# Kernel optimization log

Hardware: AMD Instinct MI355X
Metric: run time of the kernel (lower is better)

The kernel has to match this reference:

```python
import jax, jax.numpy as jnp
import numpy as np
import math

NUM_REG_TOKENS = 0  # encoder.num_register_tokens
EPS = 1e-12         # matches torch F.normalize eps


def _l2norm(x):
    # F.normalize(x, dim=-1): x / max(||x||, eps)
    n = jnp.sqrt(jnp.sum(x * x, axis=-1, keepdims=True))
    return x / jnp.maximum(n, EPS)


def setup_inputs() -> dict:
    key = jax.random.key(0)
    k1, k2 = jax.random.split(key)
    L, N, S, T, D = 3, 8, 4, 1370, 768  # 3 interested layers, T = 1 + 37^2 patches
    q_feats = jax.random.normal(k1, (L, N, T, D), dtype=jnp.float32)
    s_feats = jax.random.normal(k2, (L, N * S, T, D), dtype=jnp.float32)
    return {"q_feats": q_feats, "s_feats": s_feats}


def reference(q_feats, s_feats):
    # fuse_feature: mean over stacked interested layers
    xq = jnp.mean(q_feats, axis=0)   # [N, T, D]
    xs = jnp.mean(s_feats, axis=0)   # [N*S, T, D]
    N = xq.shape[0]
    Q = xq.shape[1] - 1 - NUM_REG_TOKENS
    side = int(math.isqrt(Q))
    # drop class (+register) tokens
    xq = xq[:, 1 + NUM_REG_TOKENS:, :]                 # [N, Q, D]
    xs = xs[:, 1 + NUM_REG_TOKENS:, :]                 # [N*S, Q, D]
    xs = xs.reshape(N, -1, xs.shape[-1])               # [N, S*Q, D]
    xq = _l2norm(xq)
    xs = _l2norm(xs)
    # cosine distance + 1-NN min over support tokens
    sim = jnp.einsum('nqd,nsd->nqs', xq, xs)           # [N, Q, S*Q]
    dist = jnp.min(1.0 - sim, axis=-1)                 # [N, Q]
    return dist.reshape(N, 1, side, side)
```

## Files before the change

kernel.cpp:

```cpp
#include <hip/hip_runtime.h>
#include <hip/hip_bf16.h>

typedef __attribute__((ext_vector_type(4))) float f32x4;
typedef __attribute__((ext_vector_type(8))) int i32x8;

#define T_TOK 1370
#define DDIM  768
#define SCV   1369
#define SCP   1408
#define MQP   1536
#define NB    8
#define NSLAB 32
#define NST   22
#define NMT   6

#define MEMFENCE asm volatile("" ::: "memory")
#define BARRIER  do { __builtin_amdgcn_s_barrier(); MEMFENCE; } while (0)
#define LGKM0    asm volatile("s_waitcnt lgkmcnt(0)" ::: "memory")

#define GLOAD_LDS16(g, l)                                                     \
  __builtin_amdgcn_global_load_lds(                                           \
      (const __attribute__((address_space(1))) unsigned int*)(g),             \
      (__attribute__((address_space(3))) unsigned int*)(l), 16, 0, 0)

extern "C" __global__ __launch_bounds__(192) void prep_kernel(
    const float* __restrict__ src, unsigned char* __restrict__ dst,
    size_t lstride)
{
  const int row  = blockIdx.x;
  const int slab = blockIdx.y;
  const int t    = threadIdx.x;
  unsigned char* drow = dst + ((size_t)slab * gridDim.x + row) * DDIM;
  if (row >= SCV) {
    reinterpret_cast<unsigned int*>(drow)[t] = 0u;
    return;
  }
  const float* base = src + ((size_t)slab * T_TOK + row + 1) * DDIM;
  float4 a = reinterpret_cast<const float4*>(base)[t];
  float4 b = reinterpret_cast<const float4*>(base + lstride)[t];
  float4 c = reinterpret_cast<const float4*>(base + 2 * lstride)[t];
  const float k3 = 1.0f / 3.0f;
  float4 m;
  m.x = (a.x + b.x + c.x) * k3;
  m.y = (a.y + b.y + c.y) * k3;
  m.z = (a.z + b.z + c.z) * k3;
  m.w = (a.w + b.w + c.w) * k3;
  float ss = m.x * m.x + m.y * m.y + m.z * m.z + m.w * m.w;
  #pragma unroll
  for (int d = 1; d < 64; d <<= 1) ss += __shfl_xor(ss, d);
  __shared__ float wsum[3];
  if ((t & 63) == 0) wsum[t >> 6] = ss;
  __syncthreads();
  float tot = wsum[0] + wsum[1] + wsum[2];
  float rn = 1.0f / fmaxf(sqrtf(tot), 1e-12f);
  int pk = __builtin_amdgcn_cvt_pk_fp8_f32(m.x * rn, m.y * rn, 0, false);
  pk = __builtin_amdgcn_cvt_pk_fp8_f32(m.z * rn, m.w * rn, pk, true);
  reinterpret_cast<unsigned int*>(drow)[t] = (unsigned int)pk;
}

extern "C" __global__ __launch_bounds__(512, 2) void simmax_kernel(
    const unsigned char* __restrict__ xq,
    const unsigned char* __restrict__ xs,
    float* __restrict__ part)
{
  const int flat = blockIdx.x;
  const int swz  = (flat & 7) * (NMT * NST) + (flat >> 3);
  const int n    = swz / (NMT * NST);
  const int idx  = swz - n * (NMT * NST);
  const int mt   = idx % NMT;
  const int st   = idx / NMT;

  const int tid  = threadIdx.x;
  const int lane = tid & 63;
  const int w    = tid >> 6;
  const int wr   = w >> 2;
  const int wcn  = w & 3;
  const int l15  = lane & 15, l4 = lane >> 4;

  __shared__ unsigned char Abuf[2][32768];
  __shared__ unsigned char Bbuf[3][32768];

  const unsigned char* gA = xq + ((size_t)n * MQP + (size_t)mt * 256) * DDIM;
  const unsigned char* gB = xs + ((size_t)n * 4 * SCP + (size_t)st * 256) * DDIM;

  int goff[4], ldso[4];
  #pragma unroll
  for (int i = 0; i < 4; ++i) {
    int c = w * 4 + i;
    int r = c * 8 + (lane >> 3);
    goff[i] = r * DDIM + (((lane & 7) ^ (r & 7)) << 4);
    ldso[i] = c * 1024;
  }

  int aoff[8], boff[4];
  #pragma unroll
  for (int mf = 0; mf < 8; ++mf) {
    int row = wr * 128 + mf * 16 + l15;
    aoff[mf] = row * 128 + ((((l4 << 1) ^ (row & 7))) << 4);
  }
  #pragma unroll
  for (int nf = 0; nf < 4; ++nf) {
    int row = wcn * 64 + nf * 16 + l15;
    boff[nf] = row * 128 + ((((l4 << 1) ^ (row & 7))) << 4);
  }

  f32x4 acc[8][4];
  {
    f32x4 zz = {0.f, 0.f, 0.f, 0.f};
    #pragma unroll
    for (int a = 0; a < 8; ++a)
      #pragma unroll
      for (int b = 0; b < 4; ++b) acc[a][b] = zz;
  }

  #define ISSUE_A(KT)                                                        \
    do {                                                                     \
      const unsigned char* ga_ = gA + (KT) * 128;                            \
      unsigned char* la_ = Abuf[(KT) & 1];                                   \
      _Pragma("unroll") for (int i = 0; i < 4; ++i)                          \
        GLOAD_LDS16(ga_ + goff[i], la_ + ldso[i]);                           \
    } while (0)
  #define ISSUE_B(KT)                                                        \
    do {                                                                     \
      const unsigned char* gb_ = gB + (KT) * 128;                            \
      unsigned char* lb_ = Bbuf[(KT) % 3];                                   \
      _Pragma("unroll") for (int i = 0; i < 4; ++i)                          \
        GLOAD_LDS16(gb_ + goff[i], lb_ + ldso[i]);                           \
    } while (0)

  #define READ_FRAG(PTR, OFF, DST)                                           \
    do {                                                                     \
      int4 lo_ = *reinterpret_cast<const int4*>((PTR) + (OFF));              \
      int4 hi_ = *reinterpret_cast<const int4*>((PTR) + ((OFF) ^ 16));       \
      DST = i32x8{lo_.x, lo_.y, lo_.z, lo_.w, hi_.x, hi_.y, hi_.z, hi_.w};   \
    } while (0)

  ISSUE_A(0);
  ISSUE_B(0);
  ISSUE_B(1);
  asm volatile("s_waitcnt vmcnt(4)" ::: "memory");
  BARRIER;

  for (int kt = 0; kt < 6; ++kt) {
    if (kt < 5) ISSUE_A(kt + 1);
    if (kt < 4) ISSUE_B(kt + 2);

    const char* Ab = reinterpret_cast<const char*>(Abuf[kt & 1]);
    const char* Bb = reinterpret_cast<const char*>(Bbuf[kt % 3]);

    i32x8 bfr[4], af0, af1;
    #pragma unroll
    for (int nf = 0; nf < 4; ++nf) READ_FRAG(Bb, boff[nf], bfr[nf]);
    READ_FRAG(Ab, aoff[0], af0);
    READ_FRAG(Ab, aoff[1], af1);
    BARRIER; LGKM0;
    __builtin_amdgcn_s_setprio(1);
    #pragma unroll
    for (int nf = 0; nf < 4; ++nf) {
      acc[0][nf] = __builtin_amdgcn_mfma_scale_f32_16x16x128_f8f6f4(
          af0, bfr[nf], acc[0][nf], 0, 0, 0, 127, 0, 127);
      acc[1][nf] = __builtin_amdgcn_mfma_scale_f32_16x16x128_f8f6f4(
          af1, bfr[nf], acc[1][nf], 0, 0, 0, 127, 0, 127);
    }
    __builtin_amdgcn_s_setprio(0);
    BARRIER;

    #pragma unroll
    for (int p = 1; p < 4; ++p) {
      i32x8 afa, afb;
      READ_FRAG(Ab, aoff[2 * p], afa);
      READ_FRAG(Ab, aoff[2 * p + 1], afb);
      if (p == 3) {
        if (kt < 4)       asm volatile("s_waitcnt vmcnt(4)" ::: "memory");
        else if (kt == 4) asm volatile("s_waitcnt vmcnt(0)" ::: "memory");
      }
      BARRIER; LGKM0;
      __builtin_amdgcn_s_setprio(1);
      #pragma unroll
      for (int nf = 0; nf < 4; ++nf) {
        acc[2 * p][nf] = __builtin_amdgcn_mfma_scale_f32_16x16x128_f8f6f4(
            afa, bfr[nf], acc[2 * p][nf], 0, 0, 0, 127, 0, 127);
        acc[2 * p + 1][nf] = __builtin_amdgcn_mfma_scale_f32_16x16x128_f8f6f4(
            afb, bfr[nf], acc[2 * p + 1][nf], 0, 0, 0, 127, 0, 127);
      }
      __builtin_amdgcn_s_setprio(0);
      BARRIER;
    }
  }

  bool colv[4];
  #pragma unroll
  for (int nf = 0; nf < 4; ++nf) {
    int col = st * 256 + wcn * 64 + nf * 16 + l15;
    int within = col - (col / SCP) * SCP;
    colv[nf] = within < SCV;
  }

  float rm[8][4];
  #pragma unroll
  for (int mf = 0; mf < 8; ++mf)
    #pragma unroll
    for (int j = 0; j < 4; ++j) {
      float v = -1e30f;
      #pragma unroll
      for (int nf = 0; nf < 4; ++nf)
        if (colv[nf]) v = fmaxf(v, acc[mf][nf][j]);
      rm[mf][j] = v;
    }

  #pragma unroll
  for (int msk = 1; msk < 16; msk <<= 1)
    #pragma unroll
    for (int mf = 0; mf < 8; ++mf)
      #pragma unroll
      for (int j = 0; j < 4; ++j)
        rm[mf][j] = fmaxf(rm[mf][j], __shfl_xor(rm[mf][j], msk));

  __syncthreads();
  float* sfold = reinterpret_cast<float*>(&Abuf[0][0]);
  if (l15 == 0) {
    #pragma unroll
    for (int mf = 0; mf < 8; ++mf)
      #pragma unroll
      for (int j = 0; j < 4; ++j) {
        int r = wr * 128 + mf * 16 + l4 * 4 + j;
        sfold[wcn * 256 + r] = rm[mf][j];
      }
  }
  __syncthreads();
  if (tid < 256) {
    float v = fmaxf(fmaxf(sfold[tid], sfold[256 + tid]),
                    fmaxf(sfold[512 + tid], sfold[768 + tid]));
    part[((size_t)n * NST + st) * MQP + (size_t)mt * 256 + tid] = v;
  }
}

extern "C" __global__ void finalize_kernel(const float* __restrict__ part,
                                           float* __restrict__ out) {
  int i = blockIdx.x * 256 + threadIdx.x;
  if (i >= NB * SCV) return;
  int n = i / SCV, q = i - n * SCV;
  const float* p = part + (size_t)n * NST * MQP + q;
  float m = p[0];
  #pragma unroll 4
  for (int g = 1; g < NST; ++g) m = fmaxf(m, p[(size_t)g * MQP]);
  out[i] = 1.0f - m;
}

extern "C" void kernel_launch(void* const* d_in, const int* in_sizes, int n_in,
                              void* d_out, int out_size, void* d_ws, size_t ws_size,
                              hipStream_t stream) {
  const float* q_feats = (const float*)d_in[0];
  const float* s_feats = (const float*)d_in[1];
  float* out = (float*)d_out;

  char* ws = (char*)d_ws;
  const size_t xq_bytes = (size_t)NB * MQP * DDIM;
  const size_t xs_bytes = (size_t)NSLAB * SCP * DDIM;
  unsigned char* xq = (unsigned char*)ws;
  unsigned char* xs = (unsigned char*)(ws + xq_bytes);
  float* part       = (float*)(ws + xq_bytes + xs_bytes);

  prep_kernel<<<dim3(MQP, NB), 192, 0, stream>>>(
      q_feats, xq, (size_t)NB * T_TOK * DDIM);
  prep_kernel<<<dim3(SCP, NSLAB), 192, 0, stream>>>(
      s_feats, xs, (size_t)NSLAB * T_TOK * DDIM);
  simmax_kernel<<<dim3(NB * NMT * NST), 512, 0, stream>>>(xq, xs, part);
  finalize_kernel<<<dim3((NB * SCV + 255) / 256), 256, 0, stream>>>(part, out);
}
```

Baseline: 193.0 us.

## Shrink query tile to 192 rows and use one barrier per k-step

The query (A) tile per block shrinks from 256 to 192 rows, so there are 8 M-tiles instead of 6. Each wave now holds 6x4 accumulators instead of 8x4, and the A LDS buffers get smaller. The k-loop is also restructured: all six A fragments are read up front and the 24 MFMAs run back-to-back, with a single vmcnt wait and barrier at the end of each k-step instead of four barrier-separated sub-phases. This aims to cut synchronization stalls and register pressure, possibly raising occupancy, at the cost of less B reuse per block, more blocks and more B reloads from memory.

```diff
diff --git a/kernel.cpp b/kernel.cpp
--- a/kernel.cpp
+++ b/kernel.cpp
@@ -12,11 +12,10 @@
 #define NB    8
 #define NSLAB 32
 #define NST   22
-#define NMT   6
+#define NMT   8
 
 #define MEMFENCE asm volatile("" ::: "memory")
 #define BARRIER  do { __builtin_amdgcn_s_barrier(); MEMFENCE; } while (0)
-#define LGKM0    asm volatile("s_waitcnt lgkmcnt(0)" ::: "memory")
 
 #define GLOAD_LDS16(g, l)                                                     \
   __builtin_amdgcn_global_load_lds(                                           \
@@ -77,25 +76,32 @@
   const int wcn  = w & 3;
   const int l15  = lane & 15, l4 = lane >> 4;
 
-  __shared__ unsigned char Abuf[2][32768];
+  __shared__ unsigned char Abuf[2][24576];
   __shared__ unsigned char Bbuf[3][32768];
 
-  const unsigned char* gA = xq + ((size_t)n * MQP + (size_t)mt * 256) * DDIM;
+  const unsigned char* gA = xq + ((size_t)n * MQP + (size_t)mt * 192) * DDIM;
   const unsigned char* gB = xs + ((size_t)n * 4 * SCP + (size_t)st * 256) * DDIM;
 
-  int goff[4], ldso[4];
+  int agoff[3], aldso[3], bgoff[4], bldso[4];
+  #pragma unroll
+  for (int i = 0; i < 3; ++i) {
+    int c = w * 3 + i;
+    int r = c * 8 + (lane >> 3);
+    agoff[i] = r * DDIM + (((lane & 7) ^ (r & 7)) << 4);
+    aldso[i] = c * 1024;
+  }
   #pragma unroll
   for (int i = 0; i < 4; ++i) {
     int c = w * 4 + i;
     int r = c * 8 + (lane >> 3);
-    goff[i] = r * DDIM + (((lane & 7) ^ (r & 7)) << 4);
-    ldso[i] = c * 1024;
-  }
-
-  int aoff[8], boff[4];
-  #pragma unroll
-  for (int mf = 0; mf < 8; ++mf) {
-    int row = wr * 128 + mf * 16 + l15;
+    bgoff[i] = r * DDIM + (((lane & 7) ^ (r & 7)) << 4);
+    bldso[i] = c * 1024;
+  }
+
+  int aoff[6], boff[4];
+  #pragma unroll
+  for (int mf = 0; mf < 6; ++mf) {
+    int row = wr * 96 + mf * 16 + l15;
     aoff[mf] = row * 128 + ((((l4 << 1) ^ (row & 7))) << 4);
   }
   #pragma unroll
@@ -104,11 +110,11 @@
     boff[nf] = row * 128 + ((((l4 << 1) ^ (row & 7))) << 4);
   }
 
-  f32x4 acc[8][4];
+  f32x4 acc[6][4];
   {
     f32x4 zz = {0.f, 0.f, 0.f, 0.f};
     #pragma unroll
-    for (int a = 0; a < 8; ++a)
+    for (int a = 0; a < 6; ++a)
       #pragma unroll
       for (int b = 0; b < 4; ++b) acc[a][b] = zz;
   }
@@ -117,15 +123,15 @@
     do {                                                                     \
       const unsigned char* ga_ = gA + (KT) * 128;                            \
       unsigned char* la_ = Abuf[(KT) & 1];                                   \
-      _Pragma("unroll") for (int i = 0; i < 4; ++i)                          \
-        GLOAD_LDS16(ga_ + goff[i], la_ + ldso[i]);                           \
+      _Pragma("unroll") for (int i = 0; i < 3; ++i)                          \
+        GLOAD_LDS16(ga_ + agoff[i], la_ + aldso[i]);                         \
     } while (0)
   #define ISSUE_B(KT)                                                        \
     do {                                                                     \
       const unsigned char* gb_ = gB + (KT) * 128;                            \
       unsigned char* lb_ = Bbuf[(KT) % 3];                                   \
       _Pragma("unroll") for (int i = 0; i < 4; ++i)                          \
-        GLOAD_LDS16(gb_ + goff[i], lb_ + ldso[i]);                           \
+        GLOAD_LDS16(gb_ + bgoff[i], lb_ + bldso[i]);                         \
     } while (0)
 
   #define READ_FRAG(PTR, OFF, DST)                                           \
@@ -137,55 +143,36 @@
 
   ISSUE_A(0);
   ISSUE_B(0);
+  MEMFENCE;
   ISSUE_B(1);
   asm volatile("s_waitcnt vmcnt(4)" ::: "memory");
   BARRIER;
 
   for (int kt = 0; kt < 6; ++kt) {
-    if (kt < 5) ISSUE_A(kt + 1);
-    if (kt < 4) ISSUE_B(kt + 2);
+    if (kt + 1 < 6) ISSUE_A(kt + 1);
+    MEMFENCE;
+    if (kt + 2 < 6) ISSUE_B(kt + 2);
 
     const char* Ab = reinterpret_cast<const char*>(Abuf[kt & 1]);
     const char* Bb = reinterpret_cast<const char*>(Bbuf[kt % 3]);
-
-    i32x8 bfr[4], af0, af1;
+    i32x8 bfr[4], af[6];
     #pragma unroll
     for (int nf = 0; nf < 4; ++nf) READ_FRAG(Bb, boff[nf], bfr[nf]);
-    READ_FRAG(Ab, aoff[0], af0);
-    READ_FRAG(Ab, aoff[1], af1);
-    BARRIER; LGKM0;
+    #pragma unroll
+    for (int mf = 0; mf < 6; ++mf) READ_FRAG(Ab, aoff[mf], af[mf]);
+
     __builtin_amdgcn_s_setprio(1);
     #pragma unroll
-    for (int nf = 0; nf < 4; ++nf) {
-      acc[0][nf] = __builtin_amdgcn_mfma_scale_f32_16x16x128_f8f6f4(
-          af0, bfr[nf], acc[0][nf], 0, 0, 0, 127, 0, 127);
-      acc[1][nf] = __builtin_amdgcn_mfma_scale_f32_16x16x128_f8f6f4(
-          af1, bfr[nf], acc[1][nf], 0, 0, 0, 127, 0, 127);
-    }
+    for (int mf = 0; mf < 6; ++mf)
+      #pragma unroll
+      for (int nf = 0; nf < 4; ++nf)
+        acc[mf][nf] = __builtin_amdgcn_mfma_scale_f32_16x16x128_f8f6f4(
+            af[mf], bfr[nf], acc[mf][nf], 0, 0, 0, 127, 0, 127);
     __builtin_amdgcn_s_setprio(0);
-    BARRIER;
-
-    #pragma unroll
-    for (int p = 1; p < 4; ++p) {
-      i32x8 afa, afb;
-      READ_FRAG(Ab, aoff[2 * p], afa);
-      READ_FRAG(Ab, aoff[2 * p + 1], afb);
-      if (p == 3) {
-        if (kt < 4)       asm volatile("s_waitcnt vmcnt(4)" ::: "memory");
-        else if (kt == 4) asm volatile("s_waitcnt vmcnt(0)" ::: "memory");
-      }
-      BARRIER; LGKM0;
-      __builtin_amdgcn_s_setprio(1);
-      #pragma unroll
-      for (int nf = 0; nf < 4; ++nf) {
-        acc[2 * p][nf] = __builtin_amdgcn_mfma_scale_f32_16x16x128_f8f6f4(
-            afa, bfr[nf], acc[2 * p][nf], 0, 0, 0, 127, 0, 127);
-        acc[2 * p + 1][nf] = __builtin_amdgcn_mfma_scale_f32_16x16x128_f8f6f4(
-            afb, bfr[nf], acc[2 * p + 1][nf], 0, 0, 0, 127, 0, 127);
-      }
-      __builtin_amdgcn_s_setprio(0);
-      BARRIER;
-    }
+
+    if (kt < 4)       asm volatile("s_waitcnt vmcnt(4)" ::: "memory");
+    else if (kt == 4) asm volatile("s_waitcnt vmcnt(0)" ::: "memory");
+    if (kt < 5) BARRIER;
   }
 
   bool colv[4];
@@ -196,9 +183,9 @@
     colv[nf] = within < SCV;
   }
 
-  float rm[8][4];
-  #pragma unroll
-  for (int mf = 0; mf < 8; ++mf)
+  float rm[6][4];
+  #pragma unroll
+  for (int mf = 0; mf < 6; ++mf)
     #pragma unroll
     for (int j = 0; j < 4; ++j) {
       float v = -1e30f;
@@ -211,7 +198,7 @@
   #pragma unroll
   for (int msk = 1; msk < 16; msk <<= 1)
     #pragma unroll
-    for (int mf = 0; mf < 8; ++mf)
+    for (int mf = 0; mf < 6; ++mf)
       #pragma unroll
       for (int j = 0; j < 4; ++j)
         rm[mf][j] = fmaxf(rm[mf][j], __shfl_xor(rm[mf][j], msk));
@@ -220,18 +207,18 @@
   float* sfold = reinterpret_cast<float*>(&Abuf[0][0]);
   if (l15 == 0) {
     #pragma unroll
-    for (int mf = 0; mf < 8; ++mf)
+    for (int mf = 0; mf < 6; ++mf)
       #pragma unroll
       for (int j = 0; j < 4; ++j) {
-        int r = wr * 128 + mf * 16 + l4 * 4 + j;
-        sfold[wcn * 256 + r] = rm[mf][j];
+        int r = wr * 96 + mf * 16 + l4 * 4 + j;
+        sfold[wcn * 192 + r] = rm[mf][j];
       }
   }
   __syncthreads();
-  if (tid < 256) {
-    float v = fmaxf(fmaxf(sfold[tid], sfold[256 + tid]),
-                    fmaxf(sfold[512 + tid], sfold[768 + tid]));
-    part[((size_t)n * NST + st) * MQP + (size_t)mt * 256 + tid] = v;
+  if (tid < 192) {
+    float v = fmaxf(fmaxf(sfold[tid], sfold[192 + tid]),
+                    fmaxf(sfold[384 + tid], sfold[576 + tid]));
+    part[((size_t)n * NST + st) * MQP + (size_t)mt * 192 + tid] = v;
   }
 }
 
```

New measurement: 191.7 us. No clear change (-0.7%).

## Merge prep launches and collapse per-k-step barriers in simmax main loop

Applied to the files above, without the earlier changes.

The two prep launches (query and support) become one kernel with a combined grid, which selects its source, destination and padding per slab, cutting one launch and its tail. In the MFMA loop, the four barrier-separated sub-phases per k-tile become a single pass that reads each A fragment just before its MFMAs, with one barrier per k-tile after the vmcnt wait. This reduces barrier and lgkm-wait stalls, but relies on the compiler scheduling LDS reads and may lose the explicit interleaving between waves. Correctness depends on the single barrier still protecting the reuse of the triple- and double-buffered LDS tiles.

```diff
diff --git a/kernel.cpp b/kernel.cpp
--- a/kernel.cpp
+++ b/kernel.cpp
@@ -16,26 +16,42 @@
 
 #define MEMFENCE asm volatile("" ::: "memory")
 #define BARRIER  do { __builtin_amdgcn_s_barrier(); MEMFENCE; } while (0)
-#define LGKM0    asm volatile("s_waitcnt lgkmcnt(0)" ::: "memory")
 
 #define GLOAD_LDS16(g, l)                                                     \
   __builtin_amdgcn_global_load_lds(                                           \
       (const __attribute__((address_space(1))) unsigned int*)(g),             \
       (__attribute__((address_space(3))) unsigned int*)(l), 16, 0, 0)
 
-extern "C" __global__ __launch_bounds__(192) void prep_kernel(
-    const float* __restrict__ src, unsigned char* __restrict__ dst,
-    size_t lstride)
+extern "C" __global__ __launch_bounds__(192) void prep_all_kernel(
+    const float* __restrict__ qf, const float* __restrict__ sf,
+    unsigned char* __restrict__ xq, unsigned char* __restrict__ xs)
 {
-  const int row  = blockIdx.x;
-  const int slab = blockIdx.y;
-  const int t    = threadIdx.x;
-  unsigned char* drow = dst + ((size_t)slab * gridDim.x + row) * DDIM;
+  const int row = blockIdx.x;
+  const int sl  = blockIdx.y;
+  const float* src;
+  unsigned char* dst;
+  size_t lstride;
+  int pad;
+  if (sl < NB) {
+    src = qf + (size_t)sl * T_TOK * DDIM;
+    dst = xq + (size_t)sl * MQP * DDIM;
+    lstride = (size_t)NB * T_TOK * DDIM;
+    pad = MQP;
+  } else {
+    const int s2 = sl - NB;
+    src = sf + (size_t)s2 * T_TOK * DDIM;
+    dst = xs + (size_t)s2 * SCP * DDIM;
+    lstride = (size_t)NSLAB * T_TOK * DDIM;
+    pad = SCP;
+  }
+  if (row >= pad) return;
+  const int t = threadIdx.x;
+  unsigned char* drow = dst + (size_t)row * DDIM;
   if (row >= SCV) {
     reinterpret_cast<unsigned int*>(drow)[t] = 0u;
     return;
   }
-  const float* base = src + ((size_t)slab * T_TOK + row + 1) * DDIM;
+  const float* base = src + (size_t)(row + 1) * DDIM;
   float4 a = reinterpret_cast<const float4*>(base)[t];
   float4 b = reinterpret_cast<const float4*>(base + lstride)[t];
   float4 c = reinterpret_cast<const float4*>(base + 2 * lstride)[t];
@@ -137,55 +153,37 @@
 
   ISSUE_A(0);
   ISSUE_B(0);
+  MEMFENCE;
   ISSUE_B(1);
   asm volatile("s_waitcnt vmcnt(4)" ::: "memory");
   BARRIER;
 
   for (int kt = 0; kt < 6; ++kt) {
-    if (kt < 5) ISSUE_A(kt + 1);
-    if (kt < 4) ISSUE_B(kt + 2);
+    if (kt + 1 < 6) ISSUE_A(kt + 1);
+    MEMFENCE;
+    if (kt + 2 < 6) ISSUE_B(kt + 2);
 
     const char* Ab = reinterpret_cast<const char*>(Abuf[kt & 1]);
     const char* Bb = reinterpret_cast<const char*>(Bbuf[kt % 3]);
-
-    i32x8 bfr[4], af0, af1;
+    i32x8 bfr[4];
     #pragma unroll
     for (int nf = 0; nf < 4; ++nf) READ_FRAG(Bb, boff[nf], bfr[nf]);
-    READ_FRAG(Ab, aoff[0], af0);
-    READ_FRAG(Ab, aoff[1], af1);
-    BARRIER; LGKM0;
+
     __builtin_amdgcn_s_setprio(1);
     #pragma unroll
-    for (int nf = 0; nf < 4; ++nf) {
-      acc[0][nf] = __builtin_amdgcn_mfma_scale_f32_16x16x128_f8f6f4(
-          af0, bfr[nf], acc[0][nf], 0, 0, 0, 127, 0, 127);
-      acc[1][nf] = __builtin_amdgcn_mfma_scale_f32_16x16x128_f8f6f4(
-          af1, bfr[nf], acc[1][nf], 0, 0, 0, 127, 0, 127);
+    for (int mf = 0; mf < 8; ++mf) {
+      i32x8 af;
+      READ_FRAG(Ab, aoff[mf], af);
+      #pragma unroll
+      for (int nf = 0; nf < 4; ++nf)
+        acc[mf][nf] = __builtin_amdgcn_mfma_scale_f32_16x16x128_f8f6f4(
+            af, bfr[nf], acc[mf][nf], 0, 0, 0, 127, 0, 127);
     }
     __builtin_amdgcn_s_setprio(0);
-    BARRIER;
-
-    #pragma unroll
-    for (int p = 1; p < 4; ++p) {
-      i32x8 afa, afb;
-      READ_FRAG(Ab, aoff[2 * p], afa);
-      READ_FRAG(Ab, aoff[2 * p + 1], afb);
-      if (p == 3) {
-        if (kt < 4)       asm volatile("s_waitcnt vmcnt(4)" ::: "memory");
-        else if (kt == 4) asm volatile("s_waitcnt vmcnt(0)" ::: "memory");
-      }
-      BARRIER; LGKM0;
-      __builtin_amdgcn_s_setprio(1);
-      #pragma unroll
-      for (int nf = 0; nf < 4; ++nf) {
-        acc[2 * p][nf] = __builtin_amdgcn_mfma_scale_f32_16x16x128_f8f6f4(
-            afa, bfr[nf], acc[2 * p][nf], 0, 0, 0, 127, 0, 127);
-        acc[2 * p + 1][nf] = __builtin_amdgcn_mfma_scale_f32_16x16x128_f8f6f4(
-            afb, bfr[nf], acc[2 * p + 1][nf], 0, 0, 0, 127, 0, 127);
-      }
-      __builtin_amdgcn_s_setprio(0);
-      BARRIER;
-    }
+
+    if (kt < 4)       asm volatile("s_waitcnt vmcnt(4)" ::: "memory");
+    else if (kt == 4) asm volatile("s_waitcnt vmcnt(0)" ::: "memory");
+    if (kt < 5) BARRIER;
   }
 
   bool colv[4];
@@ -261,10 +259,8 @@
   unsigned char* xs = (unsigned char*)(ws + xq_bytes);
   float* part       = (float*)(ws + xq_bytes + xs_bytes);
 
-  prep_kernel<<<dim3(MQP, NB), 192, 0, stream>>>(
-      q_feats, xq, (size_t)NB * T_TOK * DDIM);
-  prep_kernel<<<dim3(SCP, NSLAB), 192, 0, stream>>>(
-      s_feats, xs, (size_t)NSLAB * T_TOK * DDIM);
+  prep_all_kernel<<<dim3(MQP, NB + NSLAB), 192, 0, stream>>>(
+      q_feats, s_feats, xq, xs);
   simmax_kernel<<<dim3(NB * NMT * NST), 512, 0, stream>>>(xq, xs, part);
   finalize_kernel<<<dim3((NB * SCV + 255) / 256), 256, 0, stream>>>(part, out);
 }
```

Result: no change. 190.5 us (-1.3%).
